# Kernel optimization log

Hardware: AMD Instinct MI355X
Metric: run time of the kernel (lower is better)

Reference implementation:

```python
import jax, jax.numpy as jnp
import numpy as np

TAU = 2.0          # LIF membrane time constant (spikingjelly default)
ALPHA = 2.0        # ATan surrogate width
EPS = 1e-5         # BatchNorm eps
NUM_HEADS = 8
SCALE = 0.125

@jax.custom_vjp
def spike(x):
    return (x >= 0.0).astype(x.dtype)

def _spike_fwd(x):
    return (x >= 0.0).astype(x.dtype), x

def _spike_bwd(x, g):
    # ATan surrogate gradient (spikingjelly default)
    return (g * (ALPHA / 2.0) / (1.0 + (jnp.pi / 2.0 * ALPHA * x) ** 2),)

spike.defvjp(_spike_fwd, _spike_bwd)

def lif(x, v_th):
    # Multi-step LIF over leading time axis T; hard reset to 0, v_reset=0.
    def step(v, xt):
        h = v + (xt - v) / TAU
        s = spike(h - v_th)
        return h * (1.0 - s), s
    _, s = jax.lax.scan(step, jnp.zeros_like(x[0]), x)
    return s

def bn(x, g, b, m, v):
    # BatchNorm1d in eval mode over channel (last) dim
    return (x - m) * jax.lax.rsqrt(v + EPS) * g + b

def setup_inputs() -> dict:
    key = jax.random.key(0)
    ks = jax.random.split(key, 16)
    T, B, N, C = 4, 16, 512, 512
    s = 1.0 / np.sqrt(C)
    inp = {"x": jax.random.normal(ks[0], (T, B, N, C), jnp.float32)}
    for i, p in enumerate("qkvp"):
        inp[f"w{p}"] = jax.random.normal(ks[1 + i], (C, C), jnp.float32) * s
        inp[f"b{p}"] = jnp.zeros((C,), jnp.float32)
        inp[f"{p}_gamma"] = jnp.ones((C,), jnp.float32)
        inp[f"{p}_beta"] = jnp.zeros((C,), jnp.float32)
        inp[f"{p}_mean"] = jax.random.normal(ks[5 + i], (C,), jnp.float32) * 0.1
        inp[f"{p}_var"] = jax.random.uniform(ks[9 + i], (C,), jnp.float32, minval=0.5, maxval=1.5)
    return inp

def reference(x, wq, bq, q_gamma, q_beta, q_mean, q_var,
              wk, bk, k_gamma, k_beta, k_mean, k_var,
              wv, bv, v_gamma, v_beta, v_mean, v_var,
              wp, bp, p_gamma, p_beta, p_mean, p_var):
    T, B, N, C = x.shape
    H = NUM_HEADS
    D = C // H

    def branch(w, b, g, be, m, va):
        y = bn(x @ w.T + b, g, be, m, va)          # Linear -> BN1d (eval)
        y = lif(y, 1.0)                             # spiking activation
        return y.reshape(T, B, N, H, D).transpose(0, 1, 3, 2, 4)  # [T,B,H,N,D]

    q = branch(wq, bq, q_gamma, q_beta, q_mean, q_var)
    k = branch(wk, bk, k_gamma, k_beta, k_mean, k_var)
    v = branch(wv, bv, v_gamma, v_beta, v_mean, v_var)

    attn = jnp.einsum('tbhnd,tbhmd->tbhnm', q, k) * SCALE  # [T,B,H,N,N]
    o = jnp.einsum('tbhnm,tbhmd->tbhnd', attn, v)          # [T,B,H,N,D]
    o = o.transpose(0, 1, 3, 2, 4).reshape(T, B, N, C)
    o = lif(o, 0.5)                                        # attn_lif, v_th=0.5
    o = bn(o @ wp.T + bp, p_gamma, p_beta, p_mean, p_var)
    return lif(o, 1.0)
```

## Files before the change

### kernel.cpp

```cpp
#include <hip/hip_runtime.h>
#include <hip/hip_bf16.h>
#include <hip/hip_fp16.h>
#include <cstddef>
#include <cstdint>

#define T_ 4
#define B_ 16
#define N_ 512
#define C_ 512
#define H_ 8
#define D_ 64
#define BN_T (B_*N_)

typedef unsigned short u16;
typedef __attribute__((ext_vector_type(8))) short bf16x8;
typedef __attribute__((ext_vector_type(8))) _Float16 f16x8;
typedef __attribute__((ext_vector_type(8))) unsigned short u16x8;
typedef __attribute__((ext_vector_type(4))) float f32x4;

__device__ __forceinline__ u16 f2bf_exact(float f) {
    union { float f; unsigned u; } x; x.f = f; return (u16)(x.u >> 16);
}
__device__ __forceinline__ void split2(float f, u16& h1, u16& h2) {
    const __half a = __float2half(f);
    const float r = (f - __half2float(a)) * 2048.0f;
    const __half b = __float2half(r);
    h1 = __half_as_ushort(a); h2 = __half_as_ushort(b);
}
__device__ __forceinline__ int swz(int rr, int q) {
    return (rr << 6) + (((q ^ ((rr >> 1) & 3)) & 3) << 4);
}
__device__ __forceinline__ int SW(int row, int col) {
    return (row << 6) + (col ^ ((row & 7) << 3));
}
__device__ __forceinline__ void gload16(const void* g, void* l) {
    __builtin_amdgcn_global_load_lds(
        (const __attribute__((address_space(1))) unsigned int*)g,
        (__attribute__((address_space(3))) unsigned int*)l, 16, 0, 0);
}

__global__ __launch_bounds__(256) void k_split_x(
    const float* __restrict__ x, u16* __restrict__ x1t, u16* __restrict__ x2t)
{
    const int tile = blockIdx.x;
    const int mt = tile >> 4, kb = tile & 15;
    const int tid = threadIdx.x;
    const int rr = tid >> 1, kh = tid & 1;
    const int t = rr & 3, bn = mt * 32 + (rr >> 2);
    const float* src = x + ((size_t)t * BN_T + bn) * C_ + kb * 32 + kh * 16;
    float f[16];
    *reinterpret_cast<float4*>(f + 0)  = *reinterpret_cast<const float4*>(src + 0);
    *reinterpret_cast<float4*>(f + 4)  = *reinterpret_cast<const float4*>(src + 4);
    *reinterpret_cast<float4*>(f + 8)  = *reinterpret_cast<const float4*>(src + 8);
    *reinterpret_cast<float4*>(f + 12) = *reinterpret_cast<const float4*>(src + 12);
    char* d1 = (char*)(x1t + ((size_t)tile << 12));
    char* d2 = (char*)(x2t + ((size_t)tile << 12));
    #pragma unroll
    for (int j = 0; j < 2; ++j) {
        u16x8 p1, p2;
        #pragma unroll
        for (int e = 0; e < 8; ++e) { u16 h1, h2; split2(f[8*j+e], h1, h2); p1[e] = h1; p2[e] = h2; }
        const int q = 2 * kh + j;
        *reinterpret_cast<u16x8*>(d1 + swz(rr, q)) = p1;
        *reinterpret_cast<u16x8*>(d2 + swz(rr, q)) = p2;
    }
}

__global__ __launch_bounds__(256) void k_split_w(
    const float* __restrict__ w, u16* __restrict__ w1t, u16* __restrict__ w2t)
{
    const int tile = blockIdx.x;
    const int nt = tile >> 4, kb = tile & 15;
    const int tid = threadIdx.x;
    const int rr = tid >> 1, kh = tid & 1;
    const int c = nt * 128 + rr;
    const float* src = w + (size_t)c * C_ + kb * 32 + kh * 16;
    float f[16];
    *reinterpret_cast<float4*>(f + 0)  = *reinterpret_cast<const float4*>(src + 0);
    *reinterpret_cast<float4*>(f + 4)  = *reinterpret_cast<const float4*>(src + 4);
    *reinterpret_cast<float4*>(f + 8)  = *reinterpret_cast<const float4*>(src + 8);
    *reinterpret_cast<float4*>(f + 12) = *reinterpret_cast<const float4*>(src + 12);
    char* d1 = (char*)(w1t + ((size_t)tile << 12));
    char* d2 = (char*)(w2t + ((size_t)tile << 12));
    #pragma unroll
    for (int j = 0; j < 2; ++j) {
        u16x8 p1, p2;
        #pragma unroll
        for (int e = 0; e < 8; ++e) { u16 h1, h2; split2(f[8*j+e], h1, h2); p1[e] = h1; p2[e] = h2; }
        const int q = 2 * kh + j;
        *reinterpret_cast<u16x8*>(d1 + swz(rr, q)) = p1;
        *reinterpret_cast<u16x8*>(d2 + swz(rr, q)) = p2;
    }
}

template<int MODE>
__global__ __launch_bounds__(256, 2) void k_linear_mfma(
    const u16* __restrict__ a1t, const u16* __restrict__ a2t,
    const u16* __restrict__ w1t, const u16* __restrict__ w2t,
    const float* __restrict__ bias, const float* __restrict__ gamma,
    const float* __restrict__ beta, const float* __restrict__ mean,
    const float* __restrict__ var, void* __restrict__ outp)
{
    __shared__ u16 lds[2][4][4096];

    const int dd  = blockIdx.x;
    const int lid = (dd & 7) * 128 + (dd >> 3);
    const int mt  = lid >> 2;
    const int nt  = lid & 3;
    const int bn0 = mt * 32;
    const int c0  = nt * 128;

    const int tid = threadIdx.x;
    const int wv  = tid >> 6, lane = tid & 63;
    const int l15 = tid & 15, g = (tid & 63) >> 4;
    const int go  = wv * 2048 + lane * 16;
    const int lo  = wv * 2048;

    f32x4 accA[2][8], accB[2][8];
    #pragma unroll
    for (int rt = 0; rt < 2; ++rt)
        #pragma unroll
        for (int ct = 0; ct < 8; ++ct) { accA[rt][ct] = {0,0,0,0}; accB[rt][ct] = {0,0,0,0}; }

    const size_t abase = (size_t)mt * 16, bbase = (size_t)nt * 16;

    auto stage = [&](int buf, int kb) {
        char* L = (char*)&lds[buf][0][0];
        const char* ga1 = (const char*)(a1t + ((abase + kb) << 12)) + go;
        const char* gb1 = (const char*)(w1t + ((bbase + kb) << 12)) + go;
        const char* gb2 = (const char*)(w2t + ((bbase + kb) << 12)) + go;
        gload16(ga1,        L + lo);
        gload16(ga1 + 1024, L + lo + 1024);
        if (MODE == 0) {
            const char* ga2 = (const char*)(a2t + ((abase + kb) << 12)) + go;
            gload16(ga2,        L + 8192 + lo);
            gload16(ga2 + 1024, L + 8192 + lo + 1024);
        }
        gload16(gb1,        L + 16384 + lo);
        gload16(gb1 + 1024, L + 16384 + lo + 1024);
        gload16(gb2,        L + 24576 + lo);
        gload16(gb2 + 1024, L + 24576 + lo + 1024);
    };

    stage(0, 0);
    __syncthreads();

    #pragma unroll 1
    for (int kb = 0; kb < 16; ++kb) {
        const int buf = kb & 1;
        if (kb < 15) stage(buf ^ 1, kb + 1);
        const char* L = (const char*)&lds[buf][0][0];
        f16x8 a1[2], a2[2];
        #pragma unroll
        for (int rt = 0; rt < 2; ++rt) {
            const int rr = wv * 32 + rt * 16 + l15;
            a1[rt] = *reinterpret_cast<const f16x8*>(L + swz(rr, g));
            if (MODE == 0)
                a2[rt] = *reinterpret_cast<const f16x8*>(L + 8192 + swz(rr, g));
        }
        #pragma unroll
        for (int ct = 0; ct < 8; ++ct) {
            const int rr2 = ct * 16 + l15;
            const f16x8 b1 = *reinterpret_cast<const f16x8*>(L + 16384 + swz(rr2, g));
            const f16x8 b2 = *reinterpret_cast<const f16x8*>(L + 24576 + swz(rr2, g));
            #pragma unroll
            for (int rt = 0; rt < 2; ++rt) {
                accA[rt][ct] = __builtin_amdgcn_mfma_f32_16x16x32_f16(a1[rt], b1, accA[rt][ct], 0, 0, 0);
                if (MODE == 0)
                    accB[rt][ct] = __builtin_amdgcn_mfma_f32_16x16x32_f16(a2[rt], b1, accB[rt][ct], 0, 0, 0);
                accB[rt][ct] = __builtin_amdgcn_mfma_f32_16x16x32_f16(a1[rt], b2, accB[rt][ct], 0, 0, 0);
            }
        }
        __syncthreads();
    }

    #pragma unroll
    for (int ct = 0; ct < 8; ++ct) {
        const int c = c0 + ct * 16 + l15;
        const float rs = 1.0f / sqrtf(var[c] + 1e-5f);
        const float ga = gamma[c], be = beta[c], mu = mean[c], bi = bias[c];
        #pragma unroll
        for (int rt = 0; rt < 2; ++rt) {
            const int bn = bn0 + wv * 8 + rt * 4 + g;
            float vm = 0.f;
            #pragma unroll
            for (int r = 0; r < 4; ++r) {
                const float y = accA[rt][ct][r] + accB[rt][ct][r] * (1.0f / 2048.0f) + bi;
                const float ybn = (y - mu) * rs * ga + be;
                const float h = vm + (ybn - vm) * 0.5f;
                const bool sp = (h >= 1.0f);
                vm = sp ? 0.f : h;
                if (MODE == 0) {
                    const int b = bn >> 9, n = bn & 511;
                    const int hh = c >> 6, d2 = c & 63;
                    ((u16*)outp)[((((size_t)r * B_ + b) * H_ + hh) * N_ + n) * D_ + d2] = sp ? 0x3F80 : 0;
                } else {
                    ((float*)outp)[((size_t)r * BN_T + bn) * C_ + c] = sp ? 1.0f : 0.0f;
                }
            }
        }
    }
}

__global__ __launch_bounds__(512, 4) void k_attn_mfma(
    const u16* __restrict__ qg, const u16* __restrict__ kg,
    const u16* __restrict__ vg, u16* __restrict__ s2t)
{
    __shared__ u16 ks[2][4096];
    __shared__ u16 vts[2][4096];
    __shared__ u16 ssb[8][2][1024];

    const int id  = blockIdx.x;
    const int lid = (id & 7) * 64 + (id >> 3);
    const int bh  = lid >> 2;
    const int qt  = lid & 3;
    const int b   = bh >> 3, hh = bh & 7;

    const int tid  = threadIdx.x;
    const int w    = tid >> 6, lane = tid & 63;
    const int l15  = lane & 15, g = lane >> 4;

    const bool isK = (tid < 256);
    const int st   = isK ? tid : tid - 256;
    const int krow = st >> 4, kcol = (st & 15) * 4;
    const int vkv  = (st & 15) * 4, vd = (st >> 4) * 4;

    ushort4 pre[4];
    bf16x8 qa[2];

    f32x4 vmem[4], oacc[4];
    #pragma unroll
    for (int d0 = 0; d0 < 4; ++d0) vmem[d0] = {0,0,0,0};

    #pragma unroll 1
    for (int t = 0; t < T_; ++t) {
        const size_t base = ((size_t)t * (B_ * H_) + bh) * (size_t)(N_ * D_);

        auto prefetch = [&](int j2) {
            const int m0 = j2 * 64;
            if (isK) {
                #pragma unroll
                for (int i = 0; i < 4; ++i)
                    pre[i] = *reinterpret_cast<const ushort4*>(
                        kg + base + (size_t)(m0 + krow + 16 * i) * D_ + kcol);
            } else {
                #pragma unroll
                for (int i = 0; i < 4; ++i)
                    pre[i] = *reinterpret_cast<const ushort4*>(
                        vg + base + (size_t)(m0 + vkv + i) * D_ + vd);
            }
        };
        auto ldswrite = [&](int buf) {
            if (isK) {
                #pragma unroll
                for (int i = 0; i < 4; ++i)
                    *reinterpret_cast<ushort4*>(&ks[buf][SW(krow + 16 * i, kcol)]) = pre[i];
            } else {
                #pragma unroll
                for (int j = 0; j < 4; ++j) {
                    ushort4 wv4;
                    wv4.x = (&pre[0].x)[j]; wv4.y = (&pre[1].x)[j];
                    wv4.z = (&pre[2].x)[j]; wv4.w = (&pre[3].x)[j];
                    *reinterpret_cast<ushort4*>(&vts[buf][SW(vd + j, vkv)]) = wv4;
                }
            }
        };
        auto qk = [&](int kbuf, int sbuf) {
            u16* sb = &ssb[w][sbuf][0];
            #pragma unroll
            for (int kvt = 0; kvt < 4; ++kvt) {
                f32x4 acc = {0.f, 0.f, 0.f, 0.f};
                #pragma unroll
                for (int c = 0; c < 2; ++c) {
                    const bf16x8 kb = *reinterpret_cast<const bf16x8*>(
                        &ks[kbuf][SW(16 * kvt + l15, 32 * c + 8 * g)]);
                    acc = __builtin_amdgcn_mfma_f32_16x16x32_bf16(qa[c], kb, acc, 0, 0, 0);
                }
                #pragma unroll
                for (int r = 0; r < 4; ++r)
                    sb[SW(4 * g + r, 16 * kvt + l15)] = f2bf_exact(acc[r]);
            }
        };
        auto pv = [&](int vbuf, int sbuf) {
            const u16* sb = &ssb[w][sbuf][0];
            #pragma unroll
            for (int c = 0; c < 2; ++c) {
                const bf16x8 sa = *reinterpret_cast<const bf16x8*>(
                    &sb[SW(l15, 32 * c + 8 * g)]);
                #pragma unroll
                for (int d0 = 0; d0 < 4; ++d0) {
                    const bf16x8 vb = *reinterpret_cast<const bf16x8*>(
                        &vts[vbuf][SW(16 * d0 + l15, 32 * c + 8 * g)]);
                    oacc[d0] = __builtin_amdgcn_mfma_f32_16x16x32_bf16(sa, vb, oacc[d0], 0, 0, 0);
                }
            }
        };

        prefetch(0);
        {
            const size_t qrow = base + (size_t)(qt * 128 + 16 * w + l15) * D_;
            qa[0] = *reinterpret_cast<const bf16x8*>(qg + qrow + 8 * g);
            qa[1] = *reinterpret_cast<const bf16x8*>(qg + qrow + 32 + 8 * g);
        }
        #pragma unroll
        for (int d0 = 0; d0 < 4; ++d0) oacc[d0] = {0.f, 0.f, 0.f, 0.f};
        ldswrite(0);
        __syncthreads();
        prefetch(1);
        qk(0, 0);

        #pragma unroll 1
        for (int j = 0; j < 7; ++j) {
            ldswrite((j + 1) & 1);
            __syncthreads();
            if (j < 6) prefetch(j + 2);
            qk((j + 1) & 1, (j + 1) & 1);
            pv(j & 1, j & 1);
            __syncthreads();
        }
        pv(1, 1);

        #pragma unroll
        for (int d0 = 0; d0 < 4; ++d0) {
            const int c = hh * 64 + d0 * 16 + l15;
            const int kb2 = c >> 5, kq = (c >> 3) & 3, e = c & 7;
            #pragma unroll
            for (int r = 0; r < 4; ++r) {
                const float o = oacc[d0][r] * 0.125f;
                const float h = vmem[d0][r] + (o - vmem[d0][r]) * 0.5f;
                const bool sp = (h >= 0.5f);
                vmem[d0][r] = sp ? 0.f : h;
                const int n = qt * 128 + 16 * w + 4 * g + r;
                const int bn = b * 512 + n;
                const int mt2 = bn >> 5;
                const int rr2 = (bn & 31) * 4 + t;
                const size_t off = (((size_t)mt2 * 16 + kb2) << 13) + (rr2 << 6)
                                 + (((kq ^ ((rr2 >> 1) & 3)) & 3) << 4) + (e << 1);
                *(u16*)((char*)s2t + off) = sp ? 0x3C00 : 0;
            }
        }
    }
}

extern "C" void kernel_launch(void* const* d_in, const int* in_sizes, int n_in,
                              void* d_out, int out_size, void* d_ws, size_t ws_size,
                              hipStream_t stream)
{
    const float* x = (const float*)d_in[0];
    const float* W[4]  = {(const float*)d_in[1],  (const float*)d_in[7],  (const float*)d_in[13], (const float*)d_in[19]};
    const float* Bi[4] = {(const float*)d_in[2],  (const float*)d_in[8],  (const float*)d_in[14], (const float*)d_in[20]};
    const float* Ga[4] = {(const float*)d_in[3],  (const float*)d_in[9],  (const float*)d_in[15], (const float*)d_in[21]};
    const float* Be[4] = {(const float*)d_in[4],  (const float*)d_in[10], (const float*)d_in[16], (const float*)d_in[22]};
    const float* Mu[4] = {(const float*)d_in[5],  (const float*)d_in[11], (const float*)d_in[17], (const float*)d_in[23]};
    const float* Va[4] = {(const float*)d_in[6],  (const float*)d_in[12], (const float*)d_in[18], (const float*)d_in[24]};

    const size_t SPK = (size_t)T_ * B_ * N_ * C_;
    const size_t WSZ = (size_t)C_ * C_;
    u16* qb  = (u16*)d_ws;
    u16* kbf = qb + SPK;
    u16* vbf = kbf + SPK;
    u16* x1t = vbf + SPK;
    u16* x2t = x1t + SPK;
    u16* wt  = x2t + SPK;
    u16* s2t = x1t;

    dim3 blk(256);
    k_split_x<<<4096, blk, 0, stream>>>(x, x1t, x2t);
    for (int i = 0; i < 4; ++i)
        k_split_w<<<64, blk, 0, stream>>>(W[i], wt + (2*i) * WSZ, wt + (2*i+1) * WSZ);

    k_linear_mfma<0><<<1024, blk, 0, stream>>>(x1t, x2t, wt + 0*WSZ, wt + 1*WSZ, Bi[0], Ga[0], Be[0], Mu[0], Va[0], qb);
    k_linear_mfma<0><<<1024, blk, 0, stream>>>(x1t, x2t, wt + 2*WSZ, wt + 3*WSZ, Bi[1], Ga[1], Be[1], Mu[1], Va[1], kbf);
    k_linear_mfma<0><<<1024, blk, 0, stream>>>(x1t, x2t, wt + 4*WSZ, wt + 5*WSZ, Bi[2], Ga[2], Be[2], Mu[2], Va[2], vbf);
    k_attn_mfma<<<512, dim3(512), 0, stream>>>(qb, kbf, vbf, s2t);
    k_linear_mfma<1><<<1024, blk, 0, stream>>>(s2t, x2t, wt + 6*WSZ, wt + 7*WSZ, Bi[3], Ga[3], Be[3], Mu[3], Va[3], d_out);
}
```

Before: 323.4 us.

## Merge QKV linears into one launch and pipeline attention across timesteps

```diff
diff --git a/kernel.cpp b/kernel.cpp
--- a/kernel.cpp
+++ b/kernel.cpp
@@ -37,6 +37,12 @@
     __builtin_amdgcn_global_load_lds(
         (const __attribute__((address_space(1))) unsigned int*)g,
         (__attribute__((address_space(3))) unsigned int*)l, 16, 0, 0);
+}
+__device__ __forceinline__ void block_sync_lgkm() {
+    __builtin_amdgcn_sched_barrier(0);
+    asm volatile("s_waitcnt lgkmcnt(0)" ::: "memory");
+    __builtin_amdgcn_s_barrier();
+    __builtin_amdgcn_sched_barrier(0);
 }
 
 __global__ __launch_bounds__(256) void k_split_x(
@@ -93,15 +99,131 @@
     }
 }
 
-template<int MODE>
-__global__ __launch_bounds__(256, 2) void k_linear_mfma(
+__global__ __launch_bounds__(256, 2) void k_linear_qkv(
     const u16* __restrict__ a1t, const u16* __restrict__ a2t,
+    const u16* __restrict__ wt_base,
+    const float* __restrict__ bi0, const float* __restrict__ ga0, const float* __restrict__ be0,
+    const float* __restrict__ mu0, const float* __restrict__ va0,
+    const float* __restrict__ bi1, const float* __restrict__ ga1, const float* __restrict__ be1,
+    const float* __restrict__ mu1, const float* __restrict__ va1,
+    const float* __restrict__ bi2, const float* __restrict__ ga2, const float* __restrict__ be2,
+    const float* __restrict__ mu2, const float* __restrict__ va2,
+    u16* __restrict__ oq, u16* __restrict__ ok, u16* __restrict__ ov)
+{
+    __shared__ u16 lds[2][4][4096];
+
+    const int dd  = blockIdx.x;
+    const int lid = (dd & 7) * 384 + (dd >> 3);
+    const int mt  = lid / 12;
+    const int ntg = lid - mt * 12;
+    const int li  = ntg >> 2;
+    const int nt  = ntg & 3;
+    const int bn0 = mt * 32;
+    const int c0  = nt * 128;
+
+    const float* bias  = li == 0 ? bi0 : li == 1 ? bi1 : bi2;
+    const float* gamma = li == 0 ? ga0 : li == 1 ? ga1 : ga2;
+    const float* beta  = li == 0 ? be0 : li == 1 ? be1 : be2;
+    const float* mean  = li == 0 ? mu0 : li == 1 ? mu1 : mu2;
+    const float* var   = li == 0 ? va0 : li == 1 ? va1 : va2;
+    u16* outp = li == 0 ? oq : li == 1 ? ok : ov;
+
+    const size_t WSZ = (size_t)C_ * C_;
+    const u16* w1t = wt_base + (size_t)(2 * li) * WSZ;
+    const u16* w2t = wt_base + (size_t)(2 * li + 1) * WSZ;
+
+    const int tid = threadIdx.x;
+    const int wv  = tid >> 6, lane = tid & 63;
+    const int l15 = tid & 15, g = (tid & 63) >> 4;
+    const int go  = wv * 2048 + lane * 16;
+    const int lo  = wv * 2048;
+
+    f32x4 accA[2][8], accB[2][8];
+    #pragma unroll
+    for (int rt = 0; rt < 2; ++rt)
+        #pragma unroll
+        for (int ct = 0; ct < 8; ++ct) { accA[rt][ct] = {0,0,0,0}; accB[rt][ct] = {0,0,0,0}; }
+
+    const size_t abase = (size_t)mt * 16, bbase = (size_t)nt * 16;
+
+    auto stage = [&](int buf, int kb) {
+        char* L = (char*)&lds[buf][0][0];
+        const char* ga1p = (const char*)(a1t + ((abase + kb) << 12)) + go;
+        const char* ga2p = (const char*)(a2t + ((abase + kb) << 12)) + go;
+        const char* gb1 = (const char*)(w1t + ((bbase + kb) << 12)) + go;
+        const char* gb2 = (const char*)(w2t + ((bbase + kb) << 12)) + go;
+        gload16(ga1p,        L + lo);
+        gload16(ga1p + 1024, L + lo + 1024);
+        gload16(ga2p,        L + 8192 + lo);
+        gload16(ga2p + 1024, L + 8192 + lo + 1024);
+        gload16(gb1,        L + 16384 + lo);
+        gload16(gb1 + 1024, L + 16384 + lo + 1024);
+        gload16(gb2,        L + 24576 + lo);
+        gload16(gb2 + 1024, L + 24576 + lo + 1024);
+    };
+
+    stage(0, 0);
+    __syncthreads();
+
+    #pragma unroll 1
+    for (int kb = 0; kb < 16; ++kb) {
+        const int buf = kb & 1;
+        if (kb < 15) stage(buf ^ 1, kb + 1);
+        const char* L = (const char*)&lds[buf][0][0];
+        f16x8 a1[2], a2[2];
+        #pragma unroll
+        for (int rt = 0; rt < 2; ++rt) {
+            const int rr = wv * 32 + rt * 16 + l15;
+            a1[rt] = *reinterpret_cast<const f16x8*>(L + swz(rr, g));
+            a2[rt] = *reinterpret_cast<const f16x8*>(L + 8192 + swz(rr, g));
+        }
+        #pragma unroll
+        for (int ct = 0; ct < 8; ++ct) {
+            const int rr2 = ct * 16 + l15;
+            const f16x8 b1 = *reinterpret_cast<const f16x8*>(L + 16384 + swz(rr2, g));
+            const f16x8 b2 = *reinterpret_cast<const f16x8*>(L + 24576 + swz(rr2, g));
+            #pragma unroll
+            for (int rt = 0; rt < 2; ++rt) {
+                accA[rt][ct] = __builtin_amdgcn_mfma_f32_16x16x32_f16(a1[rt], b1, accA[rt][ct], 0, 0, 0);
+                accB[rt][ct] = __builtin_amdgcn_mfma_f32_16x16x32_f16(a2[rt], b1, accB[rt][ct], 0, 0, 0);
+                accB[rt][ct] = __builtin_amdgcn_mfma_f32_16x16x32_f16(a1[rt], b2, accB[rt][ct], 0, 0, 0);
+            }
+        }
+        __syncthreads();
+    }
+
+    #pragma unroll
+    for (int ct = 0; ct < 8; ++ct) {
+        const int c = c0 + ct * 16 + l15;
+        const float rs = 1.0f / sqrtf(var[c] + 1e-5f);
+        const float ga = gamma[c], be = beta[c], mu = mean[c], bi = bias[c];
+        #pragma unroll
+        for (int rt = 0; rt < 2; ++rt) {
+            const int bn = bn0 + wv * 8 + rt * 4 + g;
+            float vm = 0.f;
+            #pragma unroll
+            for (int r = 0; r < 4; ++r) {
+                const float y = accA[rt][ct][r] + accB[rt][ct][r] * (1.0f / 2048.0f) + bi;
+                const float ybn = (y - mu) * rs * ga + be;
+                const float h = vm + (ybn - vm) * 0.5f;
+                const bool sp = (h >= 1.0f);
+                vm = sp ? 0.f : h;
+                const int b = bn >> 9, n = bn & 511;
+                const int hh = c >> 6, d2 = c & 63;
+                outp[((((size_t)r * B_ + b) * H_ + hh) * N_ + n) * D_ + d2] = sp ? 0x3F80 : 0;
+            }
+        }
+    }
+}
+
+__global__ __launch_bounds__(256, 2) void k_linear_out(
+    const u16* __restrict__ a1t,
     const u16* __restrict__ w1t, const u16* __restrict__ w2t,
     const float* __restrict__ bias, const float* __restrict__ gamma,
     const float* __restrict__ beta, const float* __restrict__ mean,
-    const float* __restrict__ var, void* __restrict__ outp)
-{
-    __shared__ u16 lds[2][4][4096];
+    const float* __restrict__ var, float* __restrict__ outp)
+{
+    __shared__ u16 lds[2][3][4096];
 
     const int dd  = blockIdx.x;
     const int lid = (dd & 7) * 128 + (dd >> 3);
@@ -131,15 +253,10 @@
         const char* gb2 = (const char*)(w2t + ((bbase + kb) << 12)) + go;
         gload16(ga1,        L + lo);
         gload16(ga1 + 1024, L + lo + 1024);
-        if (MODE == 0) {
-            const char* ga2 = (const char*)(a2t + ((abase + kb) << 12)) + go;
-            gload16(ga2,        L + 8192 + lo);
-            gload16(ga2 + 1024, L + 8192 + lo + 1024);
-        }
-        gload16(gb1,        L + 16384 + lo);
-        gload16(gb1 + 1024, L + 16384 + lo + 1024);
-        gload16(gb2,        L + 24576 + lo);
-        gload16(gb2 + 1024, L + 24576 + lo + 1024);
+        gload16(gb1,        L + 8192 + lo);
+        gload16(gb1 + 1024, L + 8192 + lo + 1024);
+        gload16(gb2,        L + 16384 + lo);
+        gload16(gb2 + 1024, L + 16384 + lo + 1024);
     };
 
     stage(0, 0);
@@ -150,24 +267,20 @@
         const int buf = kb & 1;
         if (kb < 15) stage(buf ^ 1, kb + 1);
         const char* L = (const char*)&lds[buf][0][0];
-        f16x8 a1[2], a2[2];
+        f16x8 a1[2];
         #pragma unroll
         for (int rt = 0; rt < 2; ++rt) {
             const int rr = wv * 32 + rt * 16 + l15;
             a1[rt] = *reinterpret_cast<const f16x8*>(L + swz(rr, g));
-            if (MODE == 0)
-                a2[rt] = *reinterpret_cast<const f16x8*>(L + 8192 + swz(rr, g));
         }
         #pragma unroll
         for (int ct = 0; ct < 8; ++ct) {
             const int rr2 = ct * 16 + l15;
-            const f16x8 b1 = *reinterpret_cast<const f16x8*>(L + 16384 + swz(rr2, g));
-            const f16x8 b2 = *reinterpret_cast<const f16x8*>(L + 24576 + swz(rr2, g));
+            const f16x8 b1 = *reinterpret_cast<const f16x8*>(L + 8192 + swz(rr2, g));
+            const f16x8 b2 = *reinterpret_cast<const f16x8*>(L + 16384 + swz(rr2, g));
             #pragma unroll
             for (int rt = 0; rt < 2; ++rt) {
                 accA[rt][ct] = __builtin_amdgcn_mfma_f32_16x16x32_f16(a1[rt], b1, accA[rt][ct], 0, 0, 0);
-                if (MODE == 0)
-                    accB[rt][ct] = __builtin_amdgcn_mfma_f32_16x16x32_f16(a2[rt], b1, accB[rt][ct], 0, 0, 0);
                 accB[rt][ct] = __builtin_amdgcn_mfma_f32_16x16x32_f16(a1[rt], b2, accB[rt][ct], 0, 0, 0);
             }
         }
@@ -190,13 +303,7 @@
                 const float h = vm + (ybn - vm) * 0.5f;
                 const bool sp = (h >= 1.0f);
                 vm = sp ? 0.f : h;
-                if (MODE == 0) {
-                    const int b = bn >> 9, n = bn & 511;
-                    const int hh = c >> 6, d2 = c & 63;
-                    ((u16*)outp)[((((size_t)r * B_ + b) * H_ + hh) * N_ + n) * D_ + d2] = sp ? 0x3F80 : 0;
-                } else {
-                    ((float*)outp)[((size_t)r * BN_T + bn) * C_ + c] = sp ? 1.0f : 0.0f;
-                }
+                outp[((size_t)r * BN_T + bn) * C_ + c] = sp ? 1.0f : 0.0f;
             }
         }
     }
@@ -225,101 +332,87 @@
     const int krow = st >> 4, kcol = (st & 15) * 4;
     const int vkv  = (st & 15) * 4, vd = (st >> 4) * 4;
 
-    ushort4 pre[4];
-    bf16x8 qa[2];
-
+    ushort4 pre[2][4];
+    bf16x8 qa[2], qpre[2];
     f32x4 vmem[4], oacc[4];
     #pragma unroll
-    for (int d0 = 0; d0 < 4; ++d0) vmem[d0] = {0,0,0,0};
-
-    #pragma unroll 1
-    for (int t = 0; t < T_; ++t) {
-        const size_t base = ((size_t)t * (B_ * H_) + bh) * (size_t)(N_ * D_);
-
-        auto prefetch = [&](int j2) {
-            const int m0 = j2 * 64;
-            if (isK) {
-                #pragma unroll
-                for (int i = 0; i < 4; ++i)
-                    pre[i] = *reinterpret_cast<const ushort4*>(
-                        kg + base + (size_t)(m0 + krow + 16 * i) * D_ + kcol);
-            } else {
-                #pragma unroll
-                for (int i = 0; i < 4; ++i)
-                    pre[i] = *reinterpret_cast<const ushort4*>(
-                        vg + base + (size_t)(m0 + vkv + i) * D_ + vd);
-            }
-        };
-        auto ldswrite = [&](int buf) {
-            if (isK) {
-                #pragma unroll
-                for (int i = 0; i < 4; ++i)
-                    *reinterpret_cast<ushort4*>(&ks[buf][SW(krow + 16 * i, kcol)]) = pre[i];
-            } else {
-                #pragma unroll
-                for (int j = 0; j < 4; ++j) {
-                    ushort4 wv4;
-                    wv4.x = (&pre[0].x)[j]; wv4.y = (&pre[1].x)[j];
-                    wv4.z = (&pre[2].x)[j]; wv4.w = (&pre[3].x)[j];
-                    *reinterpret_cast<ushort4*>(&vts[buf][SW(vd + j, vkv)]) = wv4;
-                }
-            }
-        };
-        auto qk = [&](int kbuf, int sbuf) {
-            u16* sb = &ssb[w][sbuf][0];
-            #pragma unroll
-            for (int kvt = 0; kvt < 4; ++kvt) {
-                f32x4 acc = {0.f, 0.f, 0.f, 0.f};
-                #pragma unroll
-                for (int c = 0; c < 2; ++c) {
-                    const bf16x8 kb = *reinterpret_cast<const bf16x8*>(
-                        &ks[kbuf][SW(16 * kvt + l15, 32 * c + 8 * g)]);
-                    acc = __builtin_amdgcn_mfma_f32_16x16x32_bf16(qa[c], kb, acc, 0, 0, 0);
-                }
-                #pragma unroll
-                for (int r = 0; r < 4; ++r)
-                    sb[SW(4 * g + r, 16 * kvt + l15)] = f2bf_exact(acc[r]);
-            }
-        };
-        auto pv = [&](int vbuf, int sbuf) {
-            const u16* sb = &ssb[w][sbuf][0];
+    for (int d0 = 0; d0 < 4; ++d0) { vmem[d0] = {0,0,0,0}; oacc[d0] = {0,0,0,0}; }
+
+    auto prefetch = [&](int tl) {
+        const int t2 = tl >> 3, m0 = (tl & 7) * 64;
+        const size_t base2 = ((size_t)t2 * (B_ * H_) + bh) * (size_t)(N_ * D_);
+        ushort4* p = pre[tl & 1];
+        if (isK) {
+            #pragma unroll
+            for (int i = 0; i < 4; ++i)
+                p[i] = *reinterpret_cast<const ushort4*>(
+                    kg + base2 + (size_t)(m0 + krow + 16 * i) * D_ + kcol);
+        } else {
+            #pragma unroll
+            for (int i = 0; i < 4; ++i)
+                p[i] = *reinterpret_cast<const ushort4*>(
+                    vg + base2 + (size_t)(m0 + vkv + i) * D_ + vd);
+        }
+        if ((tl & 7) == 0) {
+            const size_t qrow = base2 + (size_t)(qt * 128 + 16 * w + l15) * D_;
+            qpre[0] = *reinterpret_cast<const bf16x8*>(qg + qrow + 8 * g);
+            qpre[1] = *reinterpret_cast<const bf16x8*>(qg + qrow + 32 + 8 * g);
+        }
+    };
+    auto ldswrite = [&](int tl) {
+        const int buf = tl & 1;
+        const ushort4* p = pre[buf];
+        if (isK) {
+            #pragma unroll
+            for (int i = 0; i < 4; ++i)
+                *reinterpret_cast<ushort4*>(&ks[buf][SW(krow + 16 * i, kcol)]) = p[i];
+        } else {
+            #pragma unroll
+            for (int j = 0; j < 4; ++j) {
+                ushort4 wv4;
+                wv4.x = (&p[0].x)[j]; wv4.y = (&p[1].x)[j];
+                wv4.z = (&p[2].x)[j]; wv4.w = (&p[3].x)[j];
+                *reinterpret_cast<ushort4*>(&vts[buf][SW(vd + j, vkv)]) = wv4;
+            }
+        }
+    };
+    auto qk = [&](int tl) {
+        const int buf = tl & 1;
+        u16* sb = &ssb[w][buf][0];
+        __builtin_amdgcn_s_setprio(1);
+        #pragma unroll
+        for (int kvt = 0; kvt < 4; ++kvt) {
+            f32x4 acc = {0.f, 0.f, 0.f, 0.f};
             #pragma unroll
             for (int c = 0; c < 2; ++c) {
-                const bf16x8 sa = *reinterpret_cast<const bf16x8*>(
-                    &sb[SW(l15, 32 * c + 8 * g)]);
-                #pragma unroll
-                for (int d0 = 0; d0 < 4; ++d0) {
-                    const bf16x8 vb = *reinterpret_cast<const bf16x8*>(
-                        &vts[vbuf][SW(16 * d0 + l15, 32 * c + 8 * g)]);
-                    oacc[d0] = __builtin_amdgcn_mfma_f32_16x16x32_bf16(sa, vb, oacc[d0], 0, 0, 0);
-                }
-            }
-        };
-
-        prefetch(0);
-        {
-            const size_t qrow = base + (size_t)(qt * 128 + 16 * w + l15) * D_;
-            qa[0] = *reinterpret_cast<const bf16x8*>(qg + qrow + 8 * g);
-            qa[1] = *reinterpret_cast<const bf16x8*>(qg + qrow + 32 + 8 * g);
-        }
-        #pragma unroll
-        for (int d0 = 0; d0 < 4; ++d0) oacc[d0] = {0.f, 0.f, 0.f, 0.f};
-        ldswrite(0);
-        __syncthreads();
-        prefetch(1);
-        qk(0, 0);
-
-        #pragma unroll 1
-        for (int j = 0; j < 7; ++j) {
-            ldswrite((j + 1) & 1);
-            __syncthreads();
-            if (j < 6) prefetch(j + 2);
-            qk((j + 1) & 1, (j + 1) & 1);
-            pv(j & 1, j & 1);
-            __syncthreads();
-        }
-        pv(1, 1);
-
+                const bf16x8 kb = *reinterpret_cast<const bf16x8*>(
+                    &ks[buf][SW(16 * kvt + l15, 32 * c + 8 * g)]);
+                acc = __builtin_amdgcn_mfma_f32_16x16x32_bf16(qa[c], kb, acc, 0, 0, 0);
+            }
+            #pragma unroll
+            for (int r = 0; r < 4; ++r)
+                sb[SW(4 * g + r, 16 * kvt + l15)] = f2bf_exact(acc[r]);
+        }
+        __builtin_amdgcn_s_setprio(0);
+    };
+    auto pv = [&](int tl) {
+        const int buf = tl & 1;
+        const u16* sb = &ssb[w][buf][0];
+        __builtin_amdgcn_s_setprio(1);
+        #pragma unroll
+        for (int c = 0; c < 2; ++c) {
+            const bf16x8 sa = *reinterpret_cast<const bf16x8*>(
+                &sb[SW(l15, 32 * c + 8 * g)]);
+            #pragma unroll
+            for (int d0 = 0; d0 < 4; ++d0) {
+                const bf16x8 vb = *reinterpret_cast<const bf16x8*>(
+                    &vts[buf][SW(16 * d0 + l15, 32 * c + 8 * g)]);
+                oacc[d0] = __builtin_amdgcn_mfma_f32_16x16x32_bf16(sa, vb, oacc[d0], 0, 0, 0);
+            }
+        }
+        __builtin_amdgcn_s_setprio(0);
+    };
+    auto lif = [&](int t) {
         #pragma unroll
         for (int d0 = 0; d0 < 4; ++d0) {
             const int c = hh * 64 + d0 * 16 + l15;
@@ -338,8 +431,31 @@
                                  + (((kq ^ ((rr2 >> 1) & 3)) & 3) << 4) + (e << 1);
                 *(u16*)((char*)s2t + off) = sp ? 0x3C00 : 0;
             }
-        }
-    }
+            oacc[d0] = {0.f, 0.f, 0.f, 0.f};
+        }
+    };
+
+    prefetch(0);
+    ldswrite(0);
+    prefetch(1);
+    prefetch(2);
+    qa[0] = qpre[0]; qa[1] = qpre[1];
+    block_sync_lgkm();
+    qk(0);
+
+    #pragma unroll 1
+    for (int i = 0; i < 31; ++i) {
+        ldswrite(i + 1);
+        block_sync_lgkm();
+        if (i < 29) prefetch(i + 3);
+        pv(i);
+        if ((i & 7) == 7) lif(i >> 3);
+        if (((i + 1) & 7) == 0) { qa[0] = qpre[0]; qa[1] = qpre[1]; }
+        qk(i + 1);
+        block_sync_lgkm();
+    }
+    pv(31);
+    lif(3);
 }
 
 extern "C" void kernel_launch(void* const* d_in, const int* in_sizes, int n_in,
@@ -369,9 +485,12 @@
     for (int i = 0; i < 4; ++i)
         k_split_w<<<64, blk, 0, stream>>>(W[i], wt + (2*i) * WSZ, wt + (2*i+1) * WSZ);
 
-    k_linear_mfma<0><<<1024, blk, 0, stream>>>(x1t, x2t, wt + 0*WSZ, wt + 1*WSZ, Bi[0], Ga[0], Be[0], Mu[0], Va[0], qb);
-    k_linear_mfma<0><<<1024, blk, 0, stream>>>(x1t, x2t, wt + 2*WSZ, wt + 3*WSZ, Bi[1], Ga[1], Be[1], Mu[1], Va[1], kbf);
-    k_linear_mfma<0><<<1024, blk, 0, stream>>>(x1t, x2t, wt + 4*WSZ, wt + 5*WSZ, Bi[2], Ga[2], Be[2], Mu[2], Va[2], vbf);
+    k_linear_qkv<<<3072, blk, 0, stream>>>(x1t, x2t, wt,
+        Bi[0], Ga[0], Be[0], Mu[0], Va[0],
+        Bi[1], Ga[1], Be[1], Mu[1], Va[1],
+        Bi[2], Ga[2], Be[2], Mu[2], Va[2],
+        qb, kbf, vbf);
     k_attn_mfma<<<512, dim3(512), 0, stream>>>(qb, kbf, vbf, s2t);
-    k_linear_mfma<1><<<1024, blk, 0, stream>>>(s2t, x2t, wt + 6*WSZ, wt + 7*WSZ, Bi[3], Ga[3], Be[3], Mu[3], Va[3], d_out);
-}
+    k_linear_out<<<1024, blk, 0, stream>>>(s2t, wt + 6*WSZ, wt + 7*WSZ,
+        Bi[3], Ga[3], Be[3], Mu[3], Va[3], (float*)d_out);
+}
```

Result: slower. 405.2 us (+25.3%).
